# Optimization experiments

Hardware: AMD Instinct MI355X
Metric: run time of the kernel (lower is better)

The kernel has to match this reference:

```python
import jax, jax.numpy as jnp
import numpy as np
from jax.scipy.linalg import cho_solve
from jax.scipy.special import gammaln

B, D, K = 8192, 2000, 64  # batch_size, input_dim, hidden_dim


def helmert_basis(d):
    """Orthonormal ILR balance basis (rows sum to zero), (d-1, d).
    Stand-in for sparse_balance_basis(random_linkage(d)): same algebraic
    properties (orthonormal contrast matrix), deterministic structure."""
    P = np.zeros((d - 1, d), np.float32)
    for i in range(d - 1):
        r = d - i - 1
        P[i, i] = np.sqrt(r / (r + 1.0))
        P[i, i + 1:] = -1.0 / np.sqrt(r * (r + 1.0))
    return P


def setup_inputs() -> dict:
    key = jax.random.key(0)
    ks = jax.random.split(key, 4)
    x = jax.random.randint(ks[0], (B, D), 0, 100).astype(jnp.float32)  # count data
    Psi = jnp.asarray(helmert_basis(D))                                 # (D-1, D)
    init_scale = 1e-3
    W_enc = init_scale * jax.random.normal(ks[1], (K, D - 1), jnp.float32)
    W_dec = init_scale * jax.random.normal(ks[2], (D - 1, K), jnp.float32)
    variational_logvars = jnp.zeros((K,), jnp.float32)
    log_sigma_sq = jnp.zeros((), jnp.float32)
    eta = 0.01 * jax.random.normal(ks[3], (B, D - 1), jnp.float32)
    return dict(x=x, Psi=Psi, W_enc=W_enc, W_dec=W_dec,
                variational_logvars=variational_logvars,
                log_sigma_sq=log_sigma_sq, eta=eta)


def reference(x, Psi, W_enc, W_dec, variational_logvars, log_sigma_sq, eta):
    n = Psi.shape[0]                       # D - 1
    log2pi = jnp.log(2.0 * jnp.pi)
    # ilr(imputer(x), Psi) = (Psi @ log(x+1).T).T ; Psi rows sum to 0 so closure cancels
    hx = jnp.log(x + 1.0) @ Psi.T          # (B, D-1)
    z_mean = hx @ W_enc.T                  # (B, K)
    mu = z_mean @ W_dec.T                  # (B, D-1)
    Dv = jnp.exp(variational_logvars)      # (K,)
    var = jnp.exp(log_sigma_sq)            # scalar sigma^2
    # MVN with cov = var*I + W diag(Dv) W^T via Woodbury / matrix det lemma
    M = jnp.diag(1.0 / Dv) + (W_dec.T @ W_dec) / var   # (K, K)
    L = jnp.linalg.cholesky(M)
    logdet = (n * log_sigma_sq + jnp.sum(variational_logvars)
              + 2.0 * jnp.sum(jnp.log(jnp.diag(L))))
    diff = eta - mu                        # (B, D-1)
    t = diff @ W_dec                       # (B, K)
    sol = cho_solve((L, True), t.T).T      # (B, K) = M^{-1} W^T diff
    quad = jnp.sum(diff * diff, -1) / var - jnp.sum(t * sol, -1) / (var * var)
    logit_loss = jnp.mean(-0.5 * (n * log2pi + logdet + quad))
    # standard normal prior on z_mean: mean over batch, sum over latent dims
    prior_loss = jnp.sum(jnp.mean(-0.5 * z_mean * z_mean - 0.5 * log2pi, axis=0))
    # Multinomial log-likelihood with logits = (Psi^T @ eta^T)^T = eta @ Psi
    logits = eta @ Psi                     # (B, D)
    logp = jax.nn.log_softmax(logits, axis=-1)
    mult_ll = (gammaln(jnp.sum(x, -1) + 1.0)
               - jnp.sum(gammaln(x + 1.0), -1)
               + jnp.sum(x * logp, -1))
    mult_loss = jnp.mean(mult_ll)
    return -(mult_loss + logit_loss + prior_loss)
```

## Files before the change

kernel.cpp:

```cpp
#include <hip/hip_runtime.h>
#include <math.h>


#define LOG2PI_F 1.8378770664093453f

typedef short  v8s    __attribute__((ext_vector_type(8)));
typedef short  v4s    __attribute__((ext_vector_type(4)));
typedef float  f32x4v __attribute__((ext_vector_type(4)));
typedef float  f32x4u __attribute__((ext_vector_type(4), aligned(4)));
typedef float  f32x2u __attribute__((ext_vector_type(2), aligned(4)));

#define OFF_A     0
#define OFF_C     2048
#define OFF_G     4096
#define OFF_MINV  8192
#define OFF_MISC  12288
#define OFF_WFRAG 12352
#define OFF_ZPART 143424
#define OFF_GPART OFF_ZPART
#define OFF_TPART 1192000
#define OFF_SCAN  2240576
#define OFF_PART  2502720
#define OFF_END   2503744

__device__ inline float red16(float v){
#pragma unroll
  for (int m = 1; m < 16; m <<= 1) v += __shfl_xor(v, m, 16);
  return v;
}
__device__ inline float bf2f(short s){
  union { unsigned u; float f; } v;
  v.u = ((unsigned)(unsigned short)s) << 16;
  return v.f;
}

__global__ __launch_bounds__(256) void prep2_kernel(const float* __restrict__ Psi,
    const float* __restrict__ Wenc, const float* __restrict__ Wdec,
    float* __restrict__ a_ws, float* __restrict__ c_ws,
    short* __restrict__ fr, float* __restrict__ gparts){
  __shared__ __align__(16) float shm[64 * 68];
  const int tid = threadIdx.x;
  const int blk = blockIdx.x;
  if (blk >= 96){
    int e = (blk - 96) * 256 + tid;
    float a = 0.f, c = 0.f;
    if (e < 1999){
      f32x2u v = *(const f32x2u*)(Psi + (size_t)e * 2001);
      a = v[0]; c = -v[1];
    }
    a_ws[e] = a;
    c_ws[e] = c;
    return;
  }
  if (blk < 64){
    float* scan = shm;
    const int k = blk;
    const float* wrow = Wenc + (size_t)k * 1999;
    int base = tid * 8;
    float w[8], sloc[8], av[8], cv[8];
    float run = 0.f;
#pragma unroll
    for (int u = 0; u < 8; ++u){
      int e = base + u;
      bool valid = (e < 1999);
      float wv = valid ? wrow[e] : 0.f;
      if (valid){
        f32x2u v = *(const f32x2u*)(Psi + (size_t)e * 2001);
        av[u] = v[0]; cv[u] = -v[1];
      } else { av[u] = 0.f; cv[u] = 0.f; }
      w[u] = wv;
      sloc[u] = run;
      run += cv[u] * wv;
    }
    scan[tid] = run;
    __syncthreads();
    for (int off = 1; off < 256; off <<= 1){
      float y = (tid >= off) ? scan[tid - off] : 0.f;
      __syncthreads();
      scan[tid] += y;
      __syncthreads();
    }
    float excl = scan[tid] - run;
    union { __bf16 b[8]; v8s s; } pk;
#pragma unroll
    for (int u = 0; u < 8; ++u){
      int e = base + u;
      float val = (e < 2000) ? (av[u] * w[u] - (excl + sloc[u])) : 0.f;
      pk.b[u] = (__bf16)val;
    }
    int sc = base >> 6;
    int r  = base & 63;
    int kh = r >> 5;
    int kg = r & 31;
    int tid_m = ((k >> 4) << 6) | ((kg >> 3) << 4) | (k & 15);
    *(v8s*)(fr + (size_t)sc * 8192 + kh * 2048 + tid_m * 8) = pk.s;
    return;
  }
  auto Ws = (float(*)[68])shm;
  const int sc = blk - 64;
  const int j0 = sc * 64;
#pragma unroll
  for (int i = 0; i < 16; ++i){
    int e = tid + i * 256;
    int j = e >> 6, kk = e & 63;
    Ws[j][kk] = (j0 + j < 1999) ? Wdec[(size_t)(j0 + j) * 64 + kk] : 0.f;
  }
  __syncthreads();
  {
    const int bcol = ((tid >> 6) << 4) | (tid & 15);
    const int kg = ((tid >> 4) & 3) * 8;
    union { __bf16 b[8]; v8s s; } p2, p3;
#pragma unroll
    for (int u = 0; u < 8; ++u){
      p2.b[u] = (__bf16)Ws[kg + u][bcol];
      p3.b[u] = (__bf16)Ws[32 + kg + u][bcol];
    }
    short* o = fr + (size_t)sc * 8192 + tid * 8;
    *(v8s*)(o + 4096) = p2.s;
    *(v8s*)(o + 6144) = p3.s;
  }
  int p = tid & 63;
  int qb = (tid >> 6) * 16;
  float acc[16] = {};
  for (int jj = 0; jj < 64; ++jj){
    float wp = Ws[jj][p];
    const float4 q0 = *(const float4*)&Ws[jj][qb];
    const float4 q1 = *(const float4*)&Ws[jj][qb + 4];
    const float4 q2 = *(const float4*)&Ws[jj][qb + 8];
    const float4 q3 = *(const float4*)&Ws[jj][qb + 12];
    acc[0]  = fmaf(wp, q0.x, acc[0]);  acc[1]  = fmaf(wp, q0.y, acc[1]);
    acc[2]  = fmaf(wp, q0.z, acc[2]);  acc[3]  = fmaf(wp, q0.w, acc[3]);
    acc[4]  = fmaf(wp, q1.x, acc[4]);  acc[5]  = fmaf(wp, q1.y, acc[5]);
    acc[6]  = fmaf(wp, q1.z, acc[6]);  acc[7]  = fmaf(wp, q1.w, acc[7]);
    acc[8]  = fmaf(wp, q2.x, acc[8]);  acc[9]  = fmaf(wp, q2.y, acc[9]);
    acc[10] = fmaf(wp, q2.z, acc[10]); acc[11] = fmaf(wp, q2.w, acc[11]);
    acc[12] = fmaf(wp, q3.x, acc[12]); acc[13] = fmaf(wp, q3.y, acc[13]);
    acc[14] = fmaf(wp, q3.z, acc[14]); acc[15] = fmaf(wp, q3.w, acc[15]);
  }
  float* gp = gparts + (size_t)sc * 4096 + (size_t)p * 64 + qb;
#pragma unroll
  for (int u = 0; u < 4; ++u){
    float4 o; o.x = acc[4*u]; o.y = acc[4*u+1]; o.z = acc[4*u+2]; o.w = acc[4*u+3];
    *(float4*)&gp[4*u] = o;
  }
}

__global__ __launch_bounds__(256) void gram_reduce_kernel(const float* __restrict__ gparts,
                                                          float* __restrict__ G){
  int e = blockIdx.x * 256 + threadIdx.x;
  float s = 0.f;
#pragma unroll
  for (int p = 0; p < 32; ++p) s += gparts[(size_t)p * 4096 + e];
  G[e] = s;
}

__global__ __launch_bounds__(256) void neumann_kernel(const float* __restrict__ Gws,
    const float* __restrict__ vlv, const float* __restrict__ lss,
    float* __restrict__ Minv, float* __restrict__ misc){
  __shared__ float As[64][65];
  __shared__ float A2s[64][65];
  __shared__ double dred[4][3];
  int tid = threadIdx.x;
  float var = expf(lss[0]);
  for (int e = tid; e < 4096; e += 256){
    int i = e >> 6;
    As[i][e & 63] = expf(vlv[i]) * Gws[e] / var;
  }
  __syncthreads();
  for (int e = tid; e < 4096; e += 256){
    int i = e >> 6, j = e & 63;
    float s = 0.f;
    for (int q = 0; q < 64; ++q) s = fmaf(As[i][q], As[q][j], s);
    A2s[i][j] = s;
  }
  __syncthreads();
  double t1 = 0, t2 = 0, t3 = 0;
  for (int e = tid; e < 4096; e += 256){
    int i = e >> 6, j = e & 63;
    if (i == j){ t1 += (double)As[i][i]; t2 += (double)A2s[i][i]; }
    t3 += (double)A2s[i][j] * (double)As[j][i];
  }
#pragma unroll
  for (int m = 1; m < 64; m <<= 1){
    t1 += __shfl_xor(t1, m, 64); t2 += __shfl_xor(t2, m, 64); t3 += __shfl_xor(t3, m, 64);
  }
  int wid = tid >> 6;
  if ((tid & 63) == 0){ dred[wid][0] = t1; dred[wid][1] = t2; dred[wid][2] = t3; }
  __syncthreads();
  for (int e = tid; e < 4096; e += 256){
    int i = e >> 6, j = e & 63;
    float v = ((i == j) ? 1.f : 0.f) - As[i][j] + A2s[i][j];
    Minv[e] = v * expf(vlv[j]);
  }
  if (tid == 0){
    double tr1 = 0, tr2 = 0, tr3 = 0;
    for (int w2 = 0; w2 < 4; ++w2){
      tr1 += dred[w2][0]; tr2 += dred[w2][1]; tr3 += dred[w2][2];
    }
    misc[0] = (float)(1999.0 * (double)lss[0] + tr1 - tr2 / 2.0 + tr3 / 3.0);
  }
}

__global__ __launch_bounds__(256) void mega_kernel(
    const float* __restrict__ x, const float* __restrict__ eta,
    const short* __restrict__ wfrag,
    const float* __restrict__ a_ws, const float* __restrict__ c_ws,
    short* __restrict__ zpart, short* __restrict__ tpart,
    float* __restrict__ scanw)
{
  __shared__ float lutlg[128];
  __shared__ __align__(16) float a_lds[512];
  __shared__ __align__(16) float c_lds[512];
  __shared__ __align__(16) __bf16 At[16][520];
  __shared__ __align__(16) __bf16 Ae[16][520];
  auto z_l = (float(*)[68])((unsigned char*)At);
  auto t_l = (float(*)[68])((unsigned char*)At + 4352);

  const int tid = threadIdx.x;
  const int split = blockIdx.x & 3;
  const int rowblk = blockIdx.x >> 2;
  const int b0 = rowblk * 16;
  const int ch0 = split * 8;
  const int cb0 = split * 512;
  if (tid < 128) lutlg[tid] = lgammaf((float)(tid + 1));
  for (int i = tid; i < 512; i += 256){ a_lds[i] = a_ws[cb0 + i]; c_lds[i] = c_ws[cb0 + i]; }

  const int lrow = tid >> 4;
  const int sl   = tid & 15;
  const int lq4  = sl * 4;
  const int wid  = tid >> 6, lan = tid & 63;
  const int arow = lan & 15;
  const int bcol = wid * 16 + (lan & 15);
  const int kgrp = (lan >> 4) * 8;

  f32x4v accz = {0.f, 0.f, 0.f, 0.f}, acct = {0.f, 0.f, 0.f, 0.f};
  float carry = 0.f, mOn = -3.0e38f, sOn = 0.f;
  float xdot = 0.f, sx = 0.f, sgl = 0.f, e2 = 0.f;

  const float* xs_base = x   + (size_t)(b0 + lrow) * 2000 + cb0 + lq4;
  const float* es_base = eta + (size_t)(b0 + lrow) * 1999 + cb0 + lq4;
  const short* fr_base = wfrag + (size_t)ch0 * 8192 + (size_t)tid * 8;
  const bool lastSplit = (split == 3);

  float xv[8][4], ev[8][4];
#pragma unroll
  for (int c = 0; c < 8; ++c){
    const float* xp = xs_base + c * 64;
    if (!(lastSplit && c == 7)){
      f32x4v v = *(const f32x4v*)xp;
      xv[c][0] = v[0]; xv[c][1] = v[1]; xv[c][2] = v[2]; xv[c][3] = v[3];
    } else {
#pragma unroll
      for (int u = 0; u < 4; ++u){
        int cc = cb0 + c * 64 + lq4 + u;
        xv[c][u] = (cc < 2000) ? xp[u] : 0.f;
      }
    }
  }
#pragma unroll
  for (int c = 0; c < 8; ++c){
    const float* ep = es_base + c * 64;
    if (!(lastSplit && c == 7)){
      f32x4u v = *(const f32x4u*)ep;
      ev[c][0] = v[0]; ev[c][1] = v[1]; ev[c][2] = v[2]; ev[c][3] = v[3];
    } else {
#pragma unroll
      for (int u = 0; u < 4; ++u){
        int cc = cb0 + c * 64 + lq4 + u;
        ev[c][u] = (cc < 1999) ? ep[u] : 0.f;
      }
    }
  }
  v8s WF0[2], WF1[2], WD0[2], WD1[2];
  {
    const short* fb = fr_base;
    WF0[0] = *(const v8s*)(fb);
    WF1[0] = *(const v8s*)(fb + 2048);
    WD0[0] = *(const v8s*)(fb + 4096);
    WD1[0] = *(const v8s*)(fb + 6144);
  }
#pragma unroll
  for (int c = 0; c < 8; ++c){
    union { __bf16 b[4]; unsigned long long q; } cx, ce;
#pragma unroll
    for (int u = 0; u < 4; ++u){
      cx.b[u] = (__bf16)__logf(xv[c][u] + 1.f);
      ce.b[u] = (__bf16)ev[c][u];
    }
    *(unsigned long long*)&At[lrow][c * 64 + lq4] = cx.q;
    *(unsigned long long*)&Ae[lrow][c * 64 + lq4] = ce.q;
  }
  __syncthreads();

#pragma unroll
  for (int c = 0; c < 8; ++c){
    if (c + 1 < 8){
      const short* fb = fr_base + (size_t)(c + 1) * 8192;
      WF0[(c + 1) & 1] = *(const v8s*)(fb);
      WF1[(c + 1) & 1] = *(const v8s*)(fb + 2048);
      WD0[(c + 1) & 1] = *(const v8s*)(fb + 4096);
      WD1[(c + 1) & 1] = *(const v8s*)(fb + 6144);
    }
    {
      const int cb = c * 64;
      v8s ax0 = *(const v8s*)&At[arow][cb + kgrp];
      v8s ax1 = *(const v8s*)&At[arow][cb + 32 + kgrp];
      v8s ae0 = *(const v8s*)&Ae[arow][cb + kgrp];
      v8s ae1 = *(const v8s*)&Ae[arow][cb + 32 + kgrp];
      accz = __builtin_amdgcn_mfma_f32_16x16x32_bf16(ax0, WF0[c & 1], accz, 0, 0, 0);
      accz = __builtin_amdgcn_mfma_f32_16x16x32_bf16(ax1, WF1[c & 1], accz, 0, 0, 0);
      acct = __builtin_amdgcn_mfma_f32_16x16x32_bf16(ae0, WD0[c & 1], acct, 0, 0, 0);
      acct = __builtin_amdgcn_mfma_f32_16x16x32_bf16(ae1, WD1[c & 1], acct, 0, 0, 0);
    }
    {
      const int j0g = (ch0 + c) * 64;
      const int jl  = c * 64;
      const bool guard = lastSplit && (c == 7);
      f32x4v cz = *(const f32x4v*)&c_lds[jl + lq4];
      f32x4v az = *(const f32x4v*)&a_lds[jl + lq4];
      float s0 = cz[0] * ev[c][0], s1 = cz[1] * ev[c][1];
      float s2 = cz[2] * ev[c][2], s3 = cz[3] * ev[c][3];
      float run = s0 + s1 + s2 + s3;
      float p1 = s0, p2 = s0 + s1, p3 = s0 + s1 + s2;
      float tot = run;
#pragma unroll
      for (int d = 1; d < 16; d <<= 1){
        float o = __shfl_up(tot, d, 16);
        if (sl >= d) tot += o;
      }
      float excl = tot - run;
      float base = carry + excl;
      carry += __shfl(tot, 15, 16);
      float lg0 = az[0] * ev[c][0] - base;
      float lg1 = az[1] * ev[c][1] - (base + p1);
      float lg2 = az[2] * ev[c][2] - (base + p2);
      float lg3 = az[3] * ev[c][3] - (base + p3);
      if (!guard){
        float cm = fmaxf(fmaxf(lg0, lg1), fmaxf(lg2, lg3));
        if (cm > mOn){ sOn *= __expf(mOn - cm); mOn = cm; }
        sOn += __expf(lg0 - mOn) + __expf(lg1 - mOn) + __expf(lg2 - mOn) + __expf(lg3 - mOn);
        xdot = fmaf(xv[c][0], lg0, xdot);
        xdot = fmaf(xv[c][1], lg1, xdot);
        xdot = fmaf(xv[c][2], lg2, xdot);
        xdot = fmaf(xv[c][3], lg3, xdot);
      } else {
        int nvalid = 2000 - (j0g + lq4);
        float cm = -3.0e38f;
        if (0 < nvalid) cm = fmaxf(cm, lg0);
        if (1 < nvalid) cm = fmaxf(cm, lg1);
        if (2 < nvalid) cm = fmaxf(cm, lg2);
        if (3 < nvalid) cm = fmaxf(cm, lg3);
        if (cm > mOn){ sOn *= __expf(mOn - cm); mOn = cm; }
        if (0 < nvalid){ sOn += __expf(lg0 - mOn); xdot = fmaf(xv[c][0], lg0, xdot); }
        if (1 < nvalid){ sOn += __expf(lg1 - mOn); xdot = fmaf(xv[c][1], lg1, xdot); }
        if (2 < nvalid){ sOn += __expf(lg2 - mOn); xdot = fmaf(xv[c][2], lg2, xdot); }
        if (3 < nvalid){ sOn += __expf(lg3 - mOn); xdot = fmaf(xv[c][3], lg3, xdot); }
      }
#pragma unroll
      for (int u = 0; u < 4; ++u){
        sx += xv[c][u];
        sgl += lutlg[(int)xv[c][u]];
        e2 = fmaf(ev[c][u], ev[c][u], e2);
      }
    }
  }

  xdot = red16(xdot); sx = red16(sx); sgl = red16(sgl); e2 = red16(e2);
#pragma unroll
  for (int d = 1; d < 16; d <<= 1){
    float om = __shfl_xor(mOn, d, 16);
    float os = __shfl_xor(sOn, d, 16);
    float nm = fmaxf(mOn, om);
    sOn = sOn * __expf(mOn - nm) + os * __expf(om - nm);
    mOn = nm;
  }
  __syncthreads();
  {
    int r0 = (lan >> 4) * 4;
#pragma unroll
    for (int r = 0; r < 4; ++r){
      z_l[r0 + r][bcol] = accz[r];
      t_l[r0 + r][bcol] = acct[r];
    }
  }
  __syncthreads();
  {
    size_t rb = (size_t)(split * 8192 + b0 + lrow) * 64 + lq4;
    f32x4v zv = *(const f32x4v*)&z_l[lrow][lq4];
    f32x4v tv = *(const f32x4v*)&t_l[lrow][lq4];
    union { __bf16 b[4]; unsigned long long q; } pz, pt;
#pragma unroll
    for (int u = 0; u < 4; ++u){ pz.b[u] = (__bf16)zv[u]; pt.b[u] = (__bf16)tv[u]; }
    *(unsigned long long*)&zpart[rb] = pz.q;
    *(unsigned long long*)&tpart[rb] = pt.q;
  }
  if (sl == 0){
    float* so = &scanw[(size_t)(split * 8192 + b0 + lrow) * 8];
    so[0] = carry; so[1] = mOn; so[2] = sOn; so[3] = xdot;
    so[4] = sx; so[5] = sgl; so[6] = e2;
  }
}

__global__ __launch_bounds__(256) void fixup_kernel(const short* __restrict__ zpart,
    const short* __restrict__ tpart, const float* __restrict__ scanw,
    const float* __restrict__ Gws, const float* __restrict__ Minv,
    const float* __restrict__ misc, const float* __restrict__ lss,
    double* __restrict__ part_out)
{
  __shared__ __align__(16) float z_l[16][68];
  __shared__ __align__(16) float t_l[16][68];
  __shared__ double rsum[16];
  const int tid = threadIdx.x;
  const int lrow = tid >> 4, sl = tid & 15, lq4 = sl * 4;
  const int b = blockIdx.x * 16 + lrow;

  float z4[4] = {0.f,0.f,0.f,0.f}, t4[4] = {0.f,0.f,0.f,0.f};
#pragma unroll
  for (int s = 0; s < 4; ++s){
    v4s zv = *(const v4s*)&zpart[(size_t)(s * 8192 + b) * 64 + lq4];
    v4s tv = *(const v4s*)&tpart[(size_t)(s * 8192 + b) * 64 + lq4];
#pragma unroll
    for (int u = 0; u < 4; ++u){ z4[u] += bf2f(zv[u]); t4[u] += bf2f(tv[u]); }
  }
#pragma unroll
  for (int u = 0; u < 4; ++u) z_l[lrow][lq4 + u] = z4[u];
  float zz = 0.f, tz = 0.f;
#pragma unroll
  for (int u = 0; u < 4; ++u){ zz = fmaf(z4[u], z4[u], zz); tz = fmaf(t4[u], z4[u], tz); }
  float gz[4] = {0.f, 0.f, 0.f, 0.f};
#pragma unroll 8
  for (int q = 0; q < 64; ++q){
    float zq = z_l[lrow][q];
    f32x4v g = *(const f32x4v*)&Gws[q * 64 + lq4];
#pragma unroll
    for (int u = 0; u < 4; ++u) gz[u] = fmaf(g[u], zq, gz[u]);
  }
  float zGz = 0.f;
#pragma unroll
  for (int u = 0; u < 4; ++u) zGz = fmaf(z4[u], gz[u], zGz);
  float tk[4];
#pragma unroll
  for (int u = 0; u < 4; ++u){ tk[u] = t4[u] - gz[u]; t_l[lrow][lq4 + u] = tk[u]; }
  float sol[4] = {0.f, 0.f, 0.f, 0.f};
#pragma unroll 8
  for (int q = 0; q < 64; ++q){
    float tq = t_l[lrow][q];
    f32x4v g = *(const f32x4v*)&Minv[q * 64 + lq4];
#pragma unroll
    for (int u = 0; u < 4; ++u) sol[u] = fmaf(g[u], tq, sol[u]);
  }
  float ts = 0.f;
#pragma unroll
  for (int u = 0; u < 4; ++u) ts = fmaf(tk[u], sol[u], ts);

  zz = red16(zz); tz = red16(tz); zGz = red16(zGz); ts = red16(ts);
  if (sl == 0){
    float C = 0.f, M = -3.0e38f, S = 0.f;
    float xdT = 0.f, sxT = 0.f, sglT = 0.f, e2T = 0.f;
#pragma unroll
    for (int s = 0; s < 4; ++s){
      const float* p = &scanw[(size_t)(s * 8192 + b) * 8];
      float mp = p[1] - C;
      float Ss = p[2];
      float mm = fmaxf(M, mp);
      S = S * __expf(M - mm) + Ss * __expf(mp - mm);
      M = mm;
      xdT += p[3] - C * p[4];
      sxT += p[4]; sglT += p[5]; e2T += p[6];
      C += p[0];
    }
    float lse = M + logf(S);
    float mult = lgammaf(sxT + 1.f) - sglT + xdT - sxT * lse;
    float var = expf(lss[0]);
    float logdet = misc[0];
    float diff2 = e2T - 2.f * tz + zGz;
    float quad = diff2 / var - ts / (var * var);
    float lp = -0.5f * (1999.f * LOG2PI_F + logdet + quad) - 0.5f * zz;
    rsum[lrow] = (double)mult + (double)lp;
  }
  __syncthreads();
  if (tid == 0){
    double s = 0.0;
#pragma unroll
    for (int r = 0; r < 16; ++r) s += rsum[r];
    part_out[blockIdx.x] = s;
  }
}

__global__ __launch_bounds__(256) void reduce_kernel(const double* __restrict__ part,
                                                     float* __restrict__ out){
  __shared__ double red[4];
  int tid = threadIdx.x;
  double acc = part[tid] + part[tid + 256];
#pragma unroll
  for (int m = 1; m < 64; m <<= 1) acc += __shfl_xor(acc, m, 64);
  if ((tid & 63) == 0) red[tid >> 6] = acc;
  __syncthreads();
  if (tid == 0){
    double tot = red[0] + red[1] + red[2] + red[3];
    double mean = tot / 8192.0;
    double loss = -(mean - 0.5 * 64.0 * 1.8378770664093453);
    out[0] = (float)loss;
  }
}

extern "C" void kernel_launch(void* const* d_in, const int* in_sizes, int n_in,
                              void* d_out, int out_size, void* d_ws, size_t ws_size,
                              hipStream_t stream){
  const float* x    = (const float*)d_in[0];
  const float* Psi  = (const float*)d_in[1];
  const float* Wenc = (const float*)d_in[2];
  const float* Wdec = (const float*)d_in[3];
  const float* vlv  = (const float*)d_in[4];
  const float* lss  = (const float*)d_in[5];
  const float* eta  = (const float*)d_in[6];
  float* ws = (float*)d_ws;
  float*  a_ws  = ws + OFF_A;
  float*  c_ws  = ws + OFF_C;
  float*  Gws   = ws + OFF_G;
  float*  Minv  = ws + OFF_MINV;
  float*  misc  = ws + OFF_MISC;
  short*  wfrag = (short*)(ws + OFF_WFRAG);
  float*  gpart = ws + OFF_GPART;
  short*  zpart = (short*)(ws + OFF_ZPART);
  short*  tpart = (short*)(ws + OFF_TPART);
  float*  scanw = ws + OFF_SCAN;
  double* partw = (double*)(ws + OFF_PART);

  prep2_kernel<<<104, 256, 0, stream>>>(Psi, Wenc, Wdec, a_ws, c_ws, wfrag, gpart);
  gram_reduce_kernel<<<16, 256, 0, stream>>>(gpart, Gws);
  neumann_kernel<<<1, 256, 0, stream>>>(Gws, vlv, lss, Minv, misc);
  mega_kernel<<<2048, 256, 0, stream>>>(x, eta, wfrag, a_ws, c_ws, zpart, tpart, scanw);
  fixup_kernel<<<512, 256, 0, stream>>>(zpart, tpart, scanw, Gws, Minv, misc, lss, partw);
  reduce_kernel<<<1, 256, 0, stream>>>(partw, (float*)d_out);
}
```

Measured before the change: 79.86 us.

## Split mega kernel column range eightfold and move Psi coefficient extraction to separate kernel

The main kernel now splits the 2000 columns into 8 chunks of 256 instead of 4 of 512, doubling the grid to 4096 blocks and halving LDS and register use per block. The fixup kernel now merges 8 partial z/t and scan records per row, and workspace offsets grow to hold them. Psi coefficient extraction moves out of prep2 into its own small kernel, which prep2 then reads. The aim is more occupancy and parallelism in the main pass, paid for by more partial-result traffic, more fixup work and one extra launch.

Measured after the change: 85.28 us. +6.8%, slower.

```diff
diff --git a/kernel.cpp b/kernel.cpp
--- a/kernel.cpp
+++ b/kernel.cpp
@@ -18,10 +18,10 @@
 #define OFF_WFRAG 12352
 #define OFF_ZPART 143424
 #define OFF_GPART OFF_ZPART
-#define OFF_TPART 1192000
-#define OFF_SCAN  2240576
-#define OFF_PART  2502720
-#define OFF_END   2503744
+#define OFF_TPART 2240576
+#define OFF_SCAN  4337728
+#define OFF_PART  4862016
+#define OFF_END   4863040
 
 __device__ inline float red16(float v){
 #pragma unroll
@@ -34,43 +34,40 @@
   return v.f;
 }
 
-__global__ __launch_bounds__(256) void prep2_kernel(const float* __restrict__ Psi,
-    const float* __restrict__ Wenc, const float* __restrict__ Wdec,
-    float* __restrict__ a_ws, float* __restrict__ c_ws,
-    short* __restrict__ fr, float* __restrict__ gparts){
+__global__ __launch_bounds__(256) void coef_kernel(const float* __restrict__ Psi,
+                                                   float* __restrict__ a_ws,
+                                                   float* __restrict__ c_ws){
+  int e = blockIdx.x * 256 + threadIdx.x;
+  float a = 0.f, c = 0.f;
+  if (e < 1999){
+    f32x2u v = *(const f32x2u*)(Psi + (size_t)e * 2001);
+    a = v[0]; c = -v[1];
+  }
+  a_ws[e] = a;
+  c_ws[e] = c;
+}
+
+__global__ __launch_bounds__(256) void prep2_kernel(const float* __restrict__ Wenc,
+    const float* __restrict__ Wdec, const float* __restrict__ a_ws,
+    const float* __restrict__ c_ws, short* __restrict__ fr,
+    float* __restrict__ gparts){
   __shared__ __align__(16) float shm[64 * 68];
   const int tid = threadIdx.x;
   const int blk = blockIdx.x;
-  if (blk >= 96){
-    int e = (blk - 96) * 256 + tid;
-    float a = 0.f, c = 0.f;
-    if (e < 1999){
-      f32x2u v = *(const f32x2u*)(Psi + (size_t)e * 2001);
-      a = v[0]; c = -v[1];
-    }
-    a_ws[e] = a;
-    c_ws[e] = c;
-    return;
-  }
   if (blk < 64){
     float* scan = shm;
     const int k = blk;
     const float* wrow = Wenc + (size_t)k * 1999;
     int base = tid * 8;
-    float w[8], sloc[8], av[8], cv[8];
+    float w[8], sloc[8];
     float run = 0.f;
 #pragma unroll
     for (int u = 0; u < 8; ++u){
       int e = base + u;
-      bool valid = (e < 1999);
-      float wv = valid ? wrow[e] : 0.f;
-      if (valid){
-        f32x2u v = *(const f32x2u*)(Psi + (size_t)e * 2001);
-        av[u] = v[0]; cv[u] = -v[1];
-      } else { av[u] = 0.f; cv[u] = 0.f; }
+      float wv = (e < 1999) ? wrow[e] : 0.f;
       w[u] = wv;
       sloc[u] = run;
-      run += cv[u] * wv;
+      run += c_ws[e] * wv;
     }
     scan[tid] = run;
     __syncthreads();
@@ -85,7 +82,7 @@
 #pragma unroll
     for (int u = 0; u < 8; ++u){
       int e = base + u;
-      float val = (e < 2000) ? (av[u] * w[u] - (excl + sloc[u])) : 0.f;
+      float val = (e < 2000) ? (a_ws[e] * w[u] - (excl + sloc[u])) : 0.f;
       pk.b[u] = (__bf16)val;
     }
     int sc = base >> 6;
@@ -209,21 +206,22 @@
     float* __restrict__ scanw)
 {
   __shared__ float lutlg[128];
-  __shared__ __align__(16) float a_lds[512];
-  __shared__ __align__(16) float c_lds[512];
-  __shared__ __align__(16) __bf16 At[16][520];
-  __shared__ __align__(16) __bf16 Ae[16][520];
-  auto z_l = (float(*)[68])((unsigned char*)At);
-  auto t_l = (float(*)[68])((unsigned char*)At + 4352);
+  __shared__ __align__(16) float a_lds[256];
+  __shared__ __align__(16) float c_lds[256];
+  __shared__ __align__(16) unsigned char fragbuf[16896];
+  auto At = (__bf16(*)[264])(fragbuf);
+  auto Ae = (__bf16(*)[264])(fragbuf + 8448);
+  auto z_l = (float(*)[68])(fragbuf);
+  auto t_l = (float(*)[68])(fragbuf + 4352);
 
   const int tid = threadIdx.x;
-  const int split = blockIdx.x & 3;
-  const int rowblk = blockIdx.x >> 2;
+  const int split = blockIdx.x & 7;
+  const int rowblk = blockIdx.x >> 3;
   const int b0 = rowblk * 16;
-  const int ch0 = split * 8;
-  const int cb0 = split * 512;
+  const int ch0 = split * 4;
+  const int cb0 = split * 256;
   if (tid < 128) lutlg[tid] = lgammaf((float)(tid + 1));
-  for (int i = tid; i < 512; i += 256){ a_lds[i] = a_ws[cb0 + i]; c_lds[i] = c_ws[cb0 + i]; }
+  if (tid < 256){ a_lds[tid] = a_ws[cb0 + tid]; c_lds[tid] = c_ws[cb0 + tid]; }
 
   const int lrow = tid >> 4;
   const int sl   = tid & 15;
@@ -240,13 +238,13 @@
   const float* xs_base = x   + (size_t)(b0 + lrow) * 2000 + cb0 + lq4;
   const float* es_base = eta + (size_t)(b0 + lrow) * 1999 + cb0 + lq4;
   const short* fr_base = wfrag + (size_t)ch0 * 8192 + (size_t)tid * 8;
-  const bool lastSplit = (split == 3);
-
-  float xv[8][4], ev[8][4];
-#pragma unroll
-  for (int c = 0; c < 8; ++c){
+  const bool lastSplit = (split == 7);
+
+  float xv[4][4], ev[4][4];
+#pragma unroll
+  for (int c = 0; c < 4; ++c){
     const float* xp = xs_base + c * 64;
-    if (!(lastSplit && c == 7)){
+    if (!(lastSplit && c == 3)){
       f32x4v v = *(const f32x4v*)xp;
       xv[c][0] = v[0]; xv[c][1] = v[1]; xv[c][2] = v[2]; xv[c][3] = v[3];
     } else {
@@ -258,9 +256,9 @@
     }
   }
 #pragma unroll
-  for (int c = 0; c < 8; ++c){
+  for (int c = 0; c < 4; ++c){
     const float* ep = es_base + c * 64;
-    if (!(lastSplit && c == 7)){
+    if (!(lastSplit && c == 3)){
       f32x4u v = *(const f32x4u*)ep;
       ev[c][0] = v[0]; ev[c][1] = v[1]; ev[c][2] = v[2]; ev[c][3] = v[3];
     } else {
@@ -280,7 +278,7 @@
     WD1[0] = *(const v8s*)(fb + 6144);
   }
 #pragma unroll
-  for (int c = 0; c < 8; ++c){
+  for (int c = 0; c < 4; ++c){
     union { __bf16 b[4]; unsigned long long q; } cx, ce;
 #pragma unroll
     for (int u = 0; u < 4; ++u){
@@ -293,8 +291,8 @@
   __syncthreads();
 
 #pragma unroll
-  for (int c = 0; c < 8; ++c){
-    if (c + 1 < 8){
+  for (int c = 0; c < 4; ++c){
+    if (c + 1 < 4){
       const short* fb = fr_base + (size_t)(c + 1) * 8192;
       WF0[(c + 1) & 1] = *(const v8s*)(fb);
       WF1[(c + 1) & 1] = *(const v8s*)(fb + 2048);
@@ -315,7 +313,7 @@
     {
       const int j0g = (ch0 + c) * 64;
       const int jl  = c * 64;
-      const bool guard = lastSplit && (c == 7);
+      const bool guard = lastSplit && (c == 3);
       f32x4v cz = *(const f32x4v*)&c_lds[jl + lq4];
       f32x4v az = *(const f32x4v*)&a_lds[jl + lq4];
       float s0 = cz[0] * ev[c][0], s1 = cz[1] * ev[c][1];
@@ -416,7 +414,7 @@
 
   float z4[4] = {0.f,0.f,0.f,0.f}, t4[4] = {0.f,0.f,0.f,0.f};
 #pragma unroll
-  for (int s = 0; s < 4; ++s){
+  for (int s = 0; s < 8; ++s){
     v4s zv = *(const v4s*)&zpart[(size_t)(s * 8192 + b) * 64 + lq4];
     v4s tv = *(const v4s*)&tpart[(size_t)(s * 8192 + b) * 64 + lq4];
 #pragma unroll
@@ -458,7 +456,7 @@
     float C = 0.f, M = -3.0e38f, S = 0.f;
     float xdT = 0.f, sxT = 0.f, sglT = 0.f, e2T = 0.f;
 #pragma unroll
-    for (int s = 0; s < 4; ++s){
+    for (int s = 0; s < 8; ++s){
       const float* p = &scanw[(size_t)(s * 8192 + b) * 8];
       float mp = p[1] - C;
       float Ss = p[2];
@@ -527,10 +525,11 @@
   float*  scanw = ws + OFF_SCAN;
   double* partw = (double*)(ws + OFF_PART);
 
-  prep2_kernel<<<104, 256, 0, stream>>>(Psi, Wenc, Wdec, a_ws, c_ws, wfrag, gpart);
+  coef_kernel<<<8, 256, 0, stream>>>(Psi, a_ws, c_ws);
+  prep2_kernel<<<96, 256, 0, stream>>>(Wenc, Wdec, a_ws, c_ws, wfrag, gpart);
   gram_reduce_kernel<<<16, 256, 0, stream>>>(gpart, Gws);
   neumann_kernel<<<1, 256, 0, stream>>>(Gws, vlv, lss, Minv, misc);
-  mega_kernel<<<2048, 256, 0, stream>>>(x, eta, wfrag, a_ws, c_ws, zpart, tpart, scanw);
+  mega_kernel<<<4096, 256, 0, stream>>>(x, eta, wfrag, a_ws, c_ws, zpart, tpart, scanw);
   fixup_kernel<<<512, 256, 0, stream>>>(zpart, tpart, scanw, Gws, Minv, misc, lss, partw);
   reduce_kernel<<<1, 256, 0, stream>>>(partw, (float*)d_out);
 }
```
